# Performance work log

Measured on AMD Instinct MI355X. Metric: run time of the kernel, lower is better.

## Reference

```python
import jax, jax.numpy as jnp
import numpy as np

DIM = 256
HEADS = 8
HEAD_DIM = 32
WS = 64
MLP = 1024
INNER = HEADS * HEAD_DIM
EPS = 1e-5


def setup_inputs() -> dict:
    key = jax.random.key(0)
    ks = jax.random.split(key, 10)
    B, N = 2, 65536
    s = lambda fan_in: 1.0 / np.sqrt(fan_in)
    return {
        "x": jax.random.normal(ks[0], (B, N, DIM), jnp.float32),
        "w_qkv": jax.random.normal(ks[1], (DIM, 3 * INNER), jnp.float32) * s(DIM),
        "w_out": jax.random.normal(ks[2], (INNER, DIM), jnp.float32) * s(INNER),
        "b_out": jnp.zeros((DIM,), jnp.float32),
        "pos_emb": jax.random.normal(ks[3], (WS, WS), jnp.float32),
        "ln1_g": jnp.ones((DIM,), jnp.float32),
        "ln1_b": jnp.zeros((DIM,), jnp.float32),
        "w1": jax.random.normal(ks[4], (DIM, MLP), jnp.float32) * s(DIM),
        "b1": jnp.zeros((MLP,), jnp.float32),
        "w2": jax.random.normal(ks[5], (MLP, DIM), jnp.float32) * s(MLP),
        "b2": jnp.zeros((DIM,), jnp.float32),
        "ln2_g": jnp.ones((DIM,), jnp.float32),
        "ln2_b": jnp.zeros((DIM,), jnp.float32),
    }


def layernorm(x, g, b):
    mu = jnp.mean(x, axis=-1, keepdims=True)
    var = jnp.var(x, axis=-1, keepdims=True)
    return (x - mu) * jax.lax.rsqrt(var + EPS) * g + b


def window_attn(x, w_qkv, w_out, b_out, pos_emb):
    # shifted window attention (displacement = WS // 2)
    disp = WS // 2
    x = jnp.roll(x, -disp, axis=1)
    b, n, _ = x.shape
    n_w = n // WS
    qkv = x @ w_qkv  # [b, n, 3*inner]
    qkv = qkv.reshape(b, n_w, WS, 3, HEADS, HEAD_DIM)
    q = jnp.transpose(qkv[:, :, :, 0], (0, 3, 1, 2, 4))  # [b, h, n_w, ws, d]
    k = jnp.transpose(qkv[:, :, :, 1], (0, 3, 1, 2, 4))
    v = jnp.transpose(qkv[:, :, :, 2], (0, 3, 1, 2, 4))
    scale = HEAD_DIM ** -0.5
    dots = jnp.einsum("bhwid,bhwjd->bhwij", q, k) * scale + pos_emb
    attn = jax.nn.softmax(dots, axis=-1)
    out = jnp.einsum("bhwij,bhwjd->bhwid", attn, v)
    out = jnp.transpose(out, (0, 2, 3, 1, 4)).reshape(b, n, INNER)
    out = out @ w_out + b_out
    return jnp.roll(out, disp, axis=1)


def reference(x, w_qkv, w_out, b_out, pos_emb, ln1_g, ln1_b, w1, b1, w2, b2, ln2_g, ln2_b):
    # PointSwinBlock: Residual(PreNorm(attn)) then Residual(PreNorm(ffn))
    x = x + window_attn(layernorm(x, ln1_g, ln1_b), w_qkv, w_out, b_out, pos_emb)
    h = layernorm(x, ln2_g, ln2_b)
    h = jax.nn.gelu(h @ w1 + b1, approximate=False) @ w2 + b2
    return x + h
```

## Files before the change

### kernel.cpp

```cpp
#include <hip/hip_runtime.h>
#include <hip/hip_bf16.h>
#include <math.h>
#include <stdint.h>

#define DIM   256
#define NSEQ  65536
#define NTOK  131072
#define HEADS 8
#define HD    32
#define WSZ   64
#define NWIN  2048
#define QKVN  768
#define MLPD  1024
#define LNEPS 1e-5f

typedef __bf16 bf16;
typedef __bf16 bf16x8 __attribute__((ext_vector_type(8)));
typedef __bf16 bf16x4 __attribute__((ext_vector_type(4)));
typedef float  f32x4  __attribute__((ext_vector_type(4)));

__device__ __forceinline__ int roll_row(int r) {
  return (r & 0x10000) | ((r + 32) & 0xFFFF);
}

__device__ __forceinline__ void stage16(const bf16* g, bf16* l) {
#if __has_builtin(__builtin_amdgcn_global_load_lds)
  __builtin_amdgcn_global_load_lds((const __attribute__((address_space(1))) void*)g,
                                   (__attribute__((address_space(3))) void*)l, 16, 0, 0);
#else
  int lane = threadIdx.x & 63;
  *(uint4*)((char*)l + lane * 16) = *(const uint4*)g;
#endif
}

template<int K, int LDB, bool ROLL>
__device__ __forceinline__ void gemm_tile(const bf16* __restrict__ A,
                                          const bf16* __restrict__ Bt,
                                          int mBase, int nBase,
                                          bf16* sA, bf16* sB,
                                          f32x4 acc[4][4])
{
  const int tid  = threadIdx.x;
  const int wave = tid >> 6;
  const int lane = tid & 63;
  const int slot = lane & 3;
  const int swz  = (lane >> 3) & 3;
  const int rloc = lane >> 2;
  const int chunk = ((slot ^ swz) * 8);

  int lr0 = mBase + wave * 32 + rloc;
  int lr1 = lr0 + 16;
  int ar0 = ROLL ? roll_row(lr0) : lr0;
  int ar1 = ROLL ? roll_row(lr1) : lr1;
  const bf16* gA0 = A + (size_t)ar0 * K + chunk;
  const bf16* gA1 = A + (size_t)ar1 * K + chunk;
  const bf16* gB0 = Bt + (size_t)(nBase + wave * 32 + rloc) * LDB + chunk;
  const bf16* gB1 = Bt + (size_t)(nBase + wave * 32 + rloc + 16) * LDB + chunk;

  bf16* dA0 = sA + (wave * 32 +  0) * 32;
  bf16* dA1 = sA + (wave * 32 + 16) * 32;
  bf16* dB0 = sB + (wave * 32 +  0) * 32;
  bf16* dB1 = sB + (wave * 32 + 16) * 32;

  const int m0 = (wave & 1) * 64;
  const int n0 = (wave >> 1) * 64;
  const int c    = lane & 15;
  const int quad = lane >> 4;

  int fa[4], fb[4];
#pragma unroll
  for (int t = 0; t < 4; ++t) {
    int rowA = m0 + t * 16 + c;
    fa[t] = rowA * 32 + ((quad ^ ((rowA >> 1) & 3)) * 8);
    int rowB = n0 + t * 16 + c;
    fb[t] = rowB * 32 + ((quad ^ ((rowB >> 1) & 3)) * 8);
  }

  const f32x4 fzero = {0.f, 0.f, 0.f, 0.f};
#pragma unroll
  for (int i = 0; i < 4; ++i)
#pragma unroll
    for (int j = 0; j < 4; ++j) acc[i][j] = fzero;

  for (int k0 = 0; k0 < K; k0 += 32) {
    stage16(gA0 + k0, dA0);
    stage16(gA1 + k0, dA1);
    stage16(gB0 + k0, dB0);
    stage16(gB1 + k0, dB1);
    __syncthreads();
    bf16x8 afr[4], bfr[4];
#pragma unroll
    for (int t = 0; t < 4; ++t) {
      afr[t] = *(const bf16x8*)(sA + fa[t]);
      bfr[t] = *(const bf16x8*)(sB + fb[t]);
    }
#pragma unroll
    for (int i = 0; i < 4; ++i)
#pragma unroll
      for (int j = 0; j < 4; ++j)
        acc[i][j] = __builtin_amdgcn_mfma_f32_16x16x32_bf16(afr[i], bfr[j], acc[i][j], 0, 0, 0);
    __syncthreads();
  }
}

__global__ __launch_bounds__(256) void k_prep(const float* __restrict__ wqkv,
                                              const float* __restrict__ wout,
                                              const float* __restrict__ w1,
                                              const float* __restrict__ w2,
                                              const float* __restrict__ pos,
                                              bf16* __restrict__ wqkvT, bf16* __restrict__ woutT,
                                              bf16* __restrict__ w1T, bf16* __restrict__ w2T,
                                              float* __restrict__ posP)
{
  const int total = 768 * 256 + 256 * 256 + 1024 * 256 + 256 * 1024 + 4096;
  for (int i = blockIdx.x * 256 + threadIdx.x; i < total; i += gridDim.x * 256) {
    int j = i;
    if (j < 768 * 256) { int n = j >> 8, k = j & 255; wqkvT[j] = (bf16)wqkv[k * 768 + n]; continue; }
    j -= 768 * 256;
    if (j < 256 * 256) { int n = j >> 8, k = j & 255; woutT[j] = (bf16)wout[k * 256 + n]; continue; }
    j -= 256 * 256;
    if (j < 1024 * 256) { int n = j >> 8, k = j & 255; w1T[j] = (bf16)w1[k * 1024 + n]; continue; }
    j -= 1024 * 256;
    if (j < 256 * 1024) { int n = j >> 10, k = j & 1023; w2T[j] = (bf16)w2[k * 256 + n]; continue; }
    j -= 256 * 1024;
    {
      int lane = j & 63, t = j >> 6;
      int nt = t & 3, r = (t >> 2) & 3, mt = t >> 4;
      int ii = mt * 16 + (lane >> 4) * 4 + r, jj = nt * 16 + (lane & 15);
      posP[j] = pos[ii * 64 + jj];
    }
  }
}

__global__ __launch_bounds__(256) void k_ln(const float* __restrict__ x,
                                            const float* __restrict__ gam,
                                            const float* __restrict__ bet,
                                            bf16* __restrict__ out)
{
  const int wave = threadIdx.x >> 6, lane = threadIdx.x & 63;
  const int token = blockIdx.x * 4 + wave;
  const float4 v = ((const float4*)x)[(size_t)token * 64 + lane];
  float s = v.x + v.y + v.z + v.w;
  float q = v.x * v.x + v.y * v.y + v.z * v.z + v.w * v.w;
#pragma unroll
  for (int off = 32; off; off >>= 1) { s += __shfl_xor(s, off); q += __shfl_xor(q, off); }
  const float mu = s * (1.f / 256.f);
  const float var = q * (1.f / 256.f) - mu * mu;
  const float rs = rsqrtf(var + LNEPS);
  const float4 gv = ((const float4*)gam)[lane];
  const float4 bv = ((const float4*)bet)[lane];
  bf16x4 o;
  o[0] = (bf16)((v.x - mu) * rs * gv.x + bv.x);
  o[1] = (bf16)((v.y - mu) * rs * gv.y + bv.y);
  o[2] = (bf16)((v.z - mu) * rs * gv.z + bv.z);
  o[3] = (bf16)((v.w - mu) * rs * gv.w + bv.w);
  *(bf16x4*)(out + (size_t)token * 256 + lane * 4) = o;
}

__global__ __launch_bounds__(256, 2) void k_gemm_qkv(const bf16* __restrict__ h1,
                                                     const bf16* __restrict__ wqkvT,
                                                     bf16* __restrict__ qkv)
{
  __shared__ __align__(16) bf16 sA[128 * 32];
  __shared__ __align__(16) bf16 sB[128 * 32];
  f32x4 acc[4][4];
  const int mBase = blockIdx.x * 128, nBase = blockIdx.y * 128;
  gemm_tile<256, 256, true>(h1, wqkvT, mBase, nBase, sA, sB, acc);
  const int lane = threadIdx.x & 63, wave = threadIdx.x >> 6;
  const int c = lane & 15, quad = lane >> 4;
  const int rowBase = mBase + (wave & 1) * 64 + quad * 4;
  const int colBase = nBase + (wave >> 1) * 64 + c;
#pragma unroll
  for (int i = 0; i < 4; ++i)
#pragma unroll
    for (int j = 0; j < 4; ++j)
#pragma unroll
      for (int r = 0; r < 4; ++r)
        qkv[(size_t)(rowBase + i * 16 + r) * QKVN + (colBase + j * 16)] = (bf16)acc[i][j][r];
}

__global__ __launch_bounds__(256, 2) void k_attn(const bf16* __restrict__ qkv,
                                                 const float* __restrict__ posP,
                                                 bf16* __restrict__ attn)
{
  __shared__ __align__(16) bf16 sQ[4][64 * 40];
  __shared__ __align__(16) bf16 sK[4][64 * 40];
  __shared__ __align__(16) bf16 sV[4][32 * 72];
  const int tid = threadIdx.x;
  const int wave = tid >> 6, lane = tid & 63;
  const int gh = blockIdx.y * 4 + wave;
  const int win = blockIdx.x;
  const int c = lane & 15, quad = lane >> 4;
  const size_t base = (size_t)win * 64 * QKVN;

  {
    const int row = lane >> 2;
    const int col = (lane & 3) * 8;
#pragma unroll
    for (int i = 0; i < 4; ++i) {
      int rr = i * 16 + row;
      *(uint4*)(&sQ[wave][rr * 40 + col]) = *(const uint4*)(qkv + base + (size_t)rr * QKVN + gh * 32 + col);
      *(uint4*)(&sK[wave][rr * 40 + col]) = *(const uint4*)(qkv + base + (size_t)rr * QKVN + 256 + gh * 32 + col);
    }
  }
  {
    const int d = lane & 31, jh = lane >> 5;
#pragma unroll
    for (int it = 0; it < 32; ++it) {
      int j = it * 2 + jh;
      sV[wave][d * 72 + j] = qkv[base + (size_t)j * QKVN + 512 + gh * 32 + d];
    }
  }

  const f32x4 fzero = {0.f, 0.f, 0.f, 0.f};
  f32x4 sacc[4][4];
#pragma unroll
  for (int i = 0; i < 4; ++i)
#pragma unroll
    for (int j = 0; j < 4; ++j) sacc[i][j] = fzero;
  bf16x8 qf[4], kf[4];
#pragma unroll
  for (int t = 0; t < 4; ++t) {
    qf[t] = *(const bf16x8*)(&sQ[wave][(t * 16 + c) * 40 + quad * 8]);
    kf[t] = *(const bf16x8*)(&sK[wave][(t * 16 + c) * 40 + quad * 8]);
  }
#pragma unroll
  for (int i = 0; i < 4; ++i)
#pragma unroll
    for (int j = 0; j < 4; ++j)
      sacc[i][j] = __builtin_amdgcn_mfma_f32_16x16x32_bf16(qf[i], kf[j], sacc[i][j], 0, 0, 0);

  const float scale = 0.17677669529663687f;
  float p[4][4][4];
#pragma unroll
  for (int i = 0; i < 4; ++i)
#pragma unroll
    for (int j = 0; j < 4; ++j)
#pragma unroll
      for (int r = 0; r < 4; ++r)
        p[i][j][r] = sacc[i][j][r] * scale + posP[(((i * 4 + r) * 4 + j) << 6) + lane];

  float mx[4][4], rcp[4][4];
#pragma unroll
  for (int i = 0; i < 4; ++i)
#pragma unroll
    for (int r = 0; r < 4; ++r) {
      float m = fmaxf(fmaxf(p[i][0][r], p[i][1][r]), fmaxf(p[i][2][r], p[i][3][r]));
      m = fmaxf(m, __shfl_xor(m, 1)); m = fmaxf(m, __shfl_xor(m, 2));
      m = fmaxf(m, __shfl_xor(m, 4)); m = fmaxf(m, __shfl_xor(m, 8));
      mx[i][r] = m;
    }
#pragma unroll
  for (int i = 0; i < 4; ++i)
#pragma unroll
    for (int r = 0; r < 4; ++r) {
#pragma unroll
      for (int j = 0; j < 4; ++j) p[i][j][r] = __expf(p[i][j][r] - mx[i][r]);
      float t = p[i][0][r] + p[i][1][r] + p[i][2][r] + p[i][3][r];
      t += __shfl_xor(t, 1); t += __shfl_xor(t, 2); t += __shfl_xor(t, 4); t += __shfl_xor(t, 8);
      rcp[i][r] = 1.0f / t;
    }
#pragma unroll
  for (int i = 0; i < 4; ++i)
#pragma unroll
    for (int j = 0; j < 4; ++j)
#pragma unroll
      for (int r = 0; r < 4; ++r) p[i][j][r] *= rcp[i][r];

  f32x4 oacc[4][2];
#pragma unroll
  for (int i = 0; i < 4; ++i) { oacc[i][0] = fzero; oacc[i][1] = fzero; }
#pragma unroll
  for (int half = 0; half < 2; ++half) {
#pragma unroll
    for (int i = 0; i < 4; ++i)
#pragma unroll
      for (int j2 = 0; j2 < 2; ++j2)
#pragma unroll
        for (int r = 0; r < 4; ++r)
          sQ[wave][(i * 16 + quad * 4 + r) * 40 + j2 * 16 + c] = (bf16)p[i][half * 2 + j2][r];
    bf16x8 pf[4], vf[2];
#pragma unroll
    for (int t = 0; t < 4; ++t)
      pf[t] = *(const bf16x8*)(&sQ[wave][(t * 16 + c) * 40 + quad * 8]);
#pragma unroll
    for (int n2 = 0; n2 < 2; ++n2)
      vf[n2] = *(const bf16x8*)(&sV[wave][(n2 * 16 + c) * 72 + half * 32 + quad * 8]);
#pragma unroll
    for (int i = 0; i < 4; ++i)
#pragma unroll
      for (int n2 = 0; n2 < 2; ++n2)
        oacc[i][n2] = __builtin_amdgcn_mfma_f32_16x16x32_bf16(pf[i], vf[n2], oacc[i][n2], 0, 0, 0);
  }

#pragma unroll
  for (int i = 0; i < 4; ++i)
#pragma unroll
    for (int n2 = 0; n2 < 2; ++n2)
#pragma unroll
      for (int r = 0; r < 4; ++r)
        attn[(size_t)(win * 64 + i * 16 + quad * 4 + r) * DIM + gh * 32 + n2 * 16 + c] = (bf16)oacc[i][n2][r];
}

__global__ __launch_bounds__(256, 2) void k_gemm_proj(const bf16* __restrict__ attn,
                                                      const bf16* __restrict__ woutT,
                                                      const float* __restrict__ x,
                                                      const float* __restrict__ b_out,
                                                      float* __restrict__ x2)
{
  __shared__ __align__(16) bf16 sA[128 * 32];
  __shared__ __align__(16) bf16 sB[128 * 32];
  f32x4 acc[4][4];
  const int mBase = blockIdx.x * 128, nBase = blockIdx.y * 128;
  gemm_tile<256, 256, false>(attn, woutT, mBase, nBase, sA, sB, acc);
  const int lane = threadIdx.x & 63, wave = threadIdx.x >> 6;
  const int c = lane & 15, quad = lane >> 4;
  const int rowBase = mBase + (wave & 1) * 64 + quad * 4;
  const int colBase = nBase + (wave >> 1) * 64 + c;
#pragma unroll
  for (int i = 0; i < 4; ++i)
#pragma unroll
    for (int r = 0; r < 4; ++r) {
      const int rp = rowBase + i * 16 + r;
      const size_t rowoff = (size_t)roll_row(rp) * DIM;
#pragma unroll
      for (int j = 0; j < 4; ++j) {
        const int col = colBase + j * 16;
        x2[rowoff + col] = acc[i][j][r] + b_out[col] + x[rowoff + col];
      }
    }
}

__global__ __launch_bounds__(256, 2) void k_gemm_mlp1(const bf16* __restrict__ h2,
                                                      const bf16* __restrict__ w1Th,
                                                      const float* __restrict__ b1h,
                                                      bf16* __restrict__ g)
{
  __shared__ __align__(16) bf16 sA[128 * 32];
  __shared__ __align__(16) bf16 sB[128 * 32];
  f32x4 acc[4][4];
  const int mBase = blockIdx.x * 128, nBase = blockIdx.y * 128;
  gemm_tile<256, 256, false>(h2, w1Th, mBase, nBase, sA, sB, acc);
  const int lane = threadIdx.x & 63, wave = threadIdx.x >> 6;
  const int c = lane & 15, quad = lane >> 4;
  const int rowBase = mBase + (wave & 1) * 64 + quad * 4;
  const int colBase = nBase + (wave >> 1) * 64 + c;
#pragma unroll
  for (int i = 0; i < 4; ++i)
#pragma unroll
    for (int j = 0; j < 4; ++j) {
      const int col = colBase + j * 16;
      const float bb = b1h[col];
#pragma unroll
      for (int r = 0; r < 4; ++r) {
        const float v = acc[i][j][r] + bb;
        const float ge = 0.5f * v * (1.0f + erff(v * 0.70710678118654752f));
        g[(size_t)(rowBase + i * 16 + r) * 512 + col] = (bf16)ge;
      }
    }
}

__global__ __launch_bounds__(256, 2) void k_gemm_mlp2(const bf16* __restrict__ g,
                                                      const bf16* __restrict__ w2Th,
                                                      const float* __restrict__ b2,
                                                      float* __restrict__ out,
                                                      int first)
{
  __shared__ __align__(16) bf16 sA[128 * 32];
  __shared__ __align__(16) bf16 sB[128 * 32];
  f32x4 acc[4][4];
  const int mBase = blockIdx.x * 128, nBase = blockIdx.y * 128;
  gemm_tile<512, 1024, false>(g, w2Th, mBase, nBase, sA, sB, acc);
  const int lane = threadIdx.x & 63, wave = threadIdx.x >> 6;
  const int c = lane & 15, quad = lane >> 4;
  const int rowBase = mBase + (wave & 1) * 64 + quad * 4;
  const int colBase = nBase + (wave >> 1) * 64 + c;
#pragma unroll
  for (int i = 0; i < 4; ++i)
#pragma unroll
    for (int j = 0; j < 4; ++j) {
      const int col = colBase + j * 16;
      const float bb = first ? b2[col] : 0.0f;
#pragma unroll
      for (int r = 0; r < 4; ++r) {
        const size_t off = (size_t)(rowBase + i * 16 + r) * DIM + col;
        out[off] = out[off] + acc[i][j][r] + bb;
      }
    }
}

extern "C" void kernel_launch(void* const* d_in, const int* in_sizes, int n_in,
                              void* d_out, int out_size, void* d_ws, size_t ws_size,
                              hipStream_t stream) {
  const float* x    = (const float*)d_in[0];
  const float* wqkv = (const float*)d_in[1];
  const float* wout = (const float*)d_in[2];
  const float* bo   = (const float*)d_in[3];
  const float* pos  = (const float*)d_in[4];
  const float* l1g  = (const float*)d_in[5];
  const float* l1b  = (const float*)d_in[6];
  const float* w1   = (const float*)d_in[7];
  const float* b1   = (const float*)d_in[8];
  const float* w2   = (const float*)d_in[9];
  const float* b2   = (const float*)d_in[10];
  const float* l2g  = (const float*)d_in[11];
  const float* l2b  = (const float*)d_in[12];
  float* out = (float*)d_out;

  char* ws = (char*)d_ws;
  bf16* h1   = (bf16*)ws;
  bf16* qkv  = (bf16*)(ws + 67108864);
  bf16* attn = h1;
  bf16* h2   = qkv;
  bf16* gbuf = (bf16*)(ws + 134217728);
  char* wp = ws + 268435456;
  bf16* wqkvT = (bf16*)wp;  wp += 768 * 256 * 2;
  bf16* woutT = (bf16*)wp;  wp += 256 * 256 * 2;
  bf16* w1T   = (bf16*)wp;  wp += 1024 * 256 * 2;
  bf16* w2T   = (bf16*)wp;  wp += 256 * 1024 * 2;
  float* posP = (float*)wp;

  k_prep<<<dim3(1024), dim3(256), 0, stream>>>(wqkv, wout, w1, w2, pos, wqkvT, woutT, w1T, w2T, posP);
  k_ln<<<dim3(NTOK / 4), dim3(256), 0, stream>>>(x, l1g, l1b, h1);
  k_gemm_qkv<<<dim3(1024, 6), dim3(256), 0, stream>>>(h1, wqkvT, qkv);
  k_attn<<<dim3(NWIN, 2), dim3(256), 0, stream>>>(qkv, posP, attn);
  k_gemm_proj<<<dim3(1024, 2), dim3(256), 0, stream>>>(attn, woutT, x, bo, out);
  k_ln<<<dim3(NTOK / 4), dim3(256), 0, stream>>>(out, l2g, l2b, h2);
  for (int half = 0; half < 2; ++half) {
    k_gemm_mlp1<<<dim3(1024, 4), dim3(256), 0, stream>>>(h2, w1T + half * 512 * 256, b1 + half * 512, gbuf);
    k_gemm_mlp2<<<dim3(1024, 2), dim3(256), 0, stream>>>(gbuf, w2T + half * 512, b2, out, half == 0 ? 1 : 0);
  }
}
```

Measured before the change: 946.9 us.

## Swizzle GEMM workgroups per XCD and use fast tanh-form GELU

Flattens the GEMM grids to 1D and remaps block indices so each XCD processes a contiguous range of tiles, aiming for better L2 reuse of A rows and weight tiles. Replaces the erf-based GELU with a sigmoid/exp form of the tanh approximation using a hardware reciprocal, reducing epilogue math cost. The GELU change alters numerics slightly versus the exact erf reference.

Result: faster. 863.7 us (-8.8%).

```diff
diff --git a/kernel.cpp b/kernel.cpp
--- a/kernel.cpp
+++ b/kernel.cpp
@@ -21,6 +21,23 @@
 
 __device__ __forceinline__ int roll_row(int r) {
   return (r & 0x10000) | ((r + 32) & 0xFFFF);
+}
+
+__device__ __forceinline__ float fast_gelu(float v) {
+  const float x2 = v * v;
+  const float z2 = v * __builtin_fmaf(x2, 0.07135481630268f, 1.5957691216057308f);
+  const float e  = __expf(z2);
+  const float r  = __builtin_amdgcn_rcpf(e + 1.0f);
+  return __builtin_fmaf(-v, r, v);
+}
+
+template<int NY>
+__device__ __forceinline__ void grid_swz(int& mBase, int& nBase) {
+  const int nwg  = gridDim.x;
+  const int lin  = blockIdx.x;
+  const int orig = (lin & 7) * (nwg >> 3) + (lin >> 3);
+  mBase = (orig / NY) * 128;
+  nBase = (orig % NY) * 128;
 }
 
 __device__ __forceinline__ void stage16(const bf16* g, bf16* l) {
@@ -164,7 +181,8 @@
   __shared__ __align__(16) bf16 sA[128 * 32];
   __shared__ __align__(16) bf16 sB[128 * 32];
   f32x4 acc[4][4];
-  const int mBase = blockIdx.x * 128, nBase = blockIdx.y * 128;
+  int mBase, nBase;
+  grid_swz<6>(mBase, nBase);
   gemm_tile<256, 256, true>(h1, wqkvT, mBase, nBase, sA, sB, acc);
   const int lane = threadIdx.x & 63, wave = threadIdx.x >> 6;
   const int c = lane & 15, quad = lane >> 4;
@@ -311,7 +329,8 @@
   __shared__ __align__(16) bf16 sA[128 * 32];
   __shared__ __align__(16) bf16 sB[128 * 32];
   f32x4 acc[4][4];
-  const int mBase = blockIdx.x * 128, nBase = blockIdx.y * 128;
+  int mBase, nBase;
+  grid_swz<2>(mBase, nBase);
   gemm_tile<256, 256, false>(attn, woutT, mBase, nBase, sA, sB, acc);
   const int lane = threadIdx.x & 63, wave = threadIdx.x >> 6;
   const int c = lane & 15, quad = lane >> 4;
@@ -339,7 +358,8 @@
   __shared__ __align__(16) bf16 sA[128 * 32];
   __shared__ __align__(16) bf16 sB[128 * 32];
   f32x4 acc[4][4];
-  const int mBase = blockIdx.x * 128, nBase = blockIdx.y * 128;
+  int mBase, nBase;
+  grid_swz<4>(mBase, nBase);
   gemm_tile<256, 256, false>(h2, w1Th, mBase, nBase, sA, sB, acc);
   const int lane = threadIdx.x & 63, wave = threadIdx.x >> 6;
   const int c = lane & 15, quad = lane >> 4;
@@ -354,8 +374,7 @@
 #pragma unroll
       for (int r = 0; r < 4; ++r) {
         const float v = acc[i][j][r] + bb;
-        const float ge = 0.5f * v * (1.0f + erff(v * 0.70710678118654752f));
-        g[(size_t)(rowBase + i * 16 + r) * 512 + col] = (bf16)ge;
+        g[(size_t)(rowBase + i * 16 + r) * 512 + col] = (bf16)fast_gelu(v);
       }
     }
 }
@@ -369,7 +388,8 @@
   __shared__ __align__(16) bf16 sA[128 * 32];
   __shared__ __align__(16) bf16 sB[128 * 32];
   f32x4 acc[4][4];
-  const int mBase = blockIdx.x * 128, nBase = blockIdx.y * 128;
+  int mBase, nBase;
+  grid_swz<2>(mBase, nBase);
   gemm_tile<512, 1024, false>(g, w2Th, mBase, nBase, sA, sB, acc);
   const int lane = threadIdx.x & 63, wave = threadIdx.x >> 6;
   const int c = lane & 15, quad = lane >> 4;
@@ -422,12 +442,12 @@
 
   k_prep<<<dim3(1024), dim3(256), 0, stream>>>(wqkv, wout, w1, w2, pos, wqkvT, woutT, w1T, w2T, posP);
   k_ln<<<dim3(NTOK / 4), dim3(256), 0, stream>>>(x, l1g, l1b, h1);
-  k_gemm_qkv<<<dim3(1024, 6), dim3(256), 0, stream>>>(h1, wqkvT, qkv);
+  k_gemm_qkv<<<dim3(6144), dim3(256), 0, stream>>>(h1, wqkvT, qkv);
   k_attn<<<dim3(NWIN, 2), dim3(256), 0, stream>>>(qkv, posP, attn);
-  k_gemm_proj<<<dim3(1024, 2), dim3(256), 0, stream>>>(attn, woutT, x, bo, out);
+  k_gemm_proj<<<dim3(2048), dim3(256), 0, stream>>>(attn, woutT, x, bo, out);
   k_ln<<<dim3(NTOK / 4), dim3(256), 0, stream>>>(out, l2g, l2b, h2);
   for (int half = 0; half < 2; ++half) {
-    k_gemm_mlp1<<<dim3(1024, 4), dim3(256), 0, stream>>>(h2, w1T + half * 512 * 256, b1 + half * 512, gbuf);
-    k_gemm_mlp2<<<dim3(1024, 2), dim3(256), 0, stream>>>(gbuf, w2T + half * 512, b2, out, half == 0 ? 1 : 0);
-  }
-}
+    k_gemm_mlp1<<<dim3(4096), dim3(256), 0, stream>>>(h2, w1T + half * 512 * 256, b1 + half * 512, gbuf);
+    k_gemm_mlp2<<<dim3(2048), dim3(256), 0, stream>>>(gbuf, w2T + half * 512, b2, out, half == 0 ? 1 : 0);
+  }
+}
```
